# Kernel tuning notes

Measured on AMD Instinct MI355X. Metric: run time of the kernel, lower is better.

## Reference

```python
import jax, jax.numpy as jnp
import numpy as np
from jax import lax


def _nms(heat):
    # 3x3 max-pool, stride 1, SAME padding (torch pads with -inf for max pool)
    hmax = lax.reduce_window(heat, -jnp.inf, lax.max,
                             (1, 1, 3, 3), (1, 1, 1, 1), 'SAME')
    return jnp.where(hmax == heat, heat, jnp.zeros_like(heat))


def _decode(hmap, regs, w_h_, rot, K):
    B, C, H, W = hmap.shape
    heat = _nms(jax.nn.sigmoid(hmap))
    # stage 1: per-class top-k over the H*W spatial grid
    scores_flat = heat.reshape(B, C, H * W)
    topk_scores, topk_inds = lax.top_k(scores_flat, K)          # [B, C, K]
    topk_ys = (topk_inds // W).astype(heat.dtype)
    topk_xs = (topk_inds % W).astype(heat.dtype)
    # stage 2: top-k over all C*K candidates
    topk_score, topk_ind = lax.top_k(topk_scores.reshape(B, C * K), K)  # [B, K]
    clses = (topk_ind // K).astype(heat.dtype)                   # [B, K]
    inds = jnp.take_along_axis(topk_inds.reshape(B, C * K), topk_ind, axis=1)
    ys = jnp.take_along_axis(topk_ys.reshape(B, C * K), topk_ind, axis=1)
    xs = jnp.take_along_axis(topk_xs.reshape(B, C * K), topk_ind, axis=1)

    def gather_feat(feat):  # feat: [B, ch, H, W] -> [B, K, ch]
        ch = feat.shape[1]
        f = feat.transpose(0, 2, 3, 1).reshape(B, H * W, ch)
        return jnp.take_along_axis(f, inds[:, :, None], axis=1)

    regs_g = gather_feat(regs)   # [B, K, 2]
    wh_g = gather_feat(w_h_)     # [B, K, 2]
    rot_g = gather_feat(rot)     # [B, K, 1]
    xs = xs[:, :, None] + regs_g[:, :, 0:1]
    ys = ys[:, :, None] + regs_g[:, :, 1:2]
    # detections: [x, y, w, h, rot, score, cls] -> [B, K, 7]
    return jnp.concatenate(
        [xs, ys, wh_g, rot_g, topk_score[:, :, None], clses[:, :, None]], axis=2)


def setup_inputs() -> dict:
    key = jax.random.key(0)
    k1, k2, k3, k4 = jax.random.split(key, 4)
    B, C, H, W = 1, 80, 512, 512
    return {
        'hmap': jax.random.normal(k1, (B, C, H, W), dtype=jnp.float32),
        'regs': jax.random.normal(k2, (B, 2, H, W), dtype=jnp.float32),
        'w_h_': jax.random.uniform(k3, (B, 2, H, W), dtype=jnp.float32) * 64.0,
        'rot': jax.random.normal(k4, (B, 1, H, W), dtype=jnp.float32),
        'K': 100,
    }


def reference(hmap, regs, w_h_, rot, K):
    return _decode(hmap, regs, w_h_, rot, K)
```

## Files before the change

kernel.cpp:

```cpp
#include <hip/hip_runtime.h>
#include <cstdint>

#define HH 512
#define WW 512
#define HWSZ (HH * WW)
#define TILE_H 16
#define NSEG 128
#define SEGPAD 16
#define SEGCAP 256
#define FCAP 4096
#define T0F 3.75f
#define BINBASE 8248u
#define NVB 1024

__device__ __forceinline__ float sigmoid_f(float x) {
    return 1.0f / (1.0f + expf(-x));
}

__device__ __forceinline__ uint32_t vbin(uint32_t key) {
    uint32_t b = (key >> 17) - BINBASE;
    return b > (NVB - 1) ? (NVB - 1) : b;
}

__global__ __launch_bounds__(64) void main_pass(const float* __restrict__ hmap,
                                                int nTiles,
                                                uint32_t* __restrict__ segCount,
                                                uint2* __restrict__ cand) {
    int t = blockIdx.x;
    if (t >= nTiles) return;
    const int lane = threadIdx.x;
    const int cls = t >> 5;
    const int ty = t & 31;
    const int y0 = ty * TILE_H;
    const float* base = hmap + (size_t)cls * HWSZ;
    const int xA = lane * 4;
    const int xB = 256 + lane * 4;
    const int seg = t & (NSEG - 1);
    const float NEG = -__builtin_inff();

    float4 a0, a1, a2, b0, b1, b2;
    int rm1 = (y0 > 0) ? y0 - 1 : 0;
    a0 = *(const float4*)(base + rm1 * WW + xA);
    b0 = *(const float4*)(base + rm1 * WW + xB);
    a1 = *(const float4*)(base + y0 * WW + xA);
    b1 = *(const float4*)(base + y0 * WW + xB);

    #pragma unroll
    for (int r = 0; r < TILE_H; ++r) {
        int j = y0 + 1 + r;
        int jc = (j < HH) ? j : HH - 1;
        a2 = *(const float4*)(base + jc * WW + xA);
        b2 = *(const float4*)(base + jc * WW + xB);

        float cA = fmaxf(fmaxf(a1.x, a1.y), fmaxf(a1.z, a1.w));
        float cB = fmaxf(fmaxf(b1.x, b1.y), fmaxf(b1.z, b1.w));
        if (__any(fmaxf(cA, cB) >= T0F)) {
            float4 vA, vB;
            vA.x = fmaxf(fmaxf(a0.x, a1.x), a2.x);
            vA.y = fmaxf(fmaxf(a0.y, a1.y), a2.y);
            vA.z = fmaxf(fmaxf(a0.z, a1.z), a2.z);
            vA.w = fmaxf(fmaxf(a0.w, a1.w), a2.w);
            vB.x = fmaxf(fmaxf(b0.x, b1.x), b2.x);
            vB.y = fmaxf(fmaxf(b0.y, b1.y), b2.y);
            vB.z = fmaxf(fmaxf(b0.z, b1.z), b2.z);
            vB.w = fmaxf(fmaxf(b0.w, b1.w), b2.w);
            float vAl = __shfl_up(vA.w, 1);
            float vAr = __shfl_down(vA.x, 1);
            float vBl = __shfl_up(vB.w, 1);
            float vBr = __shfl_down(vB.x, 1);
            float seamR = __shfl(vB.x, 0);
            float seamL = __shfl(vA.w, 63);
            if (lane == 0)  { vAl = NEG; vBl = seamL; }
            if (lane == 63) { vAr = seamR; vBr = NEG; }
            float mA0 = fmaxf(fmaxf(vAl, vA.x), vA.y);
            float mA1 = fmaxf(fmaxf(vA.x, vA.y), vA.z);
            float mA2 = fmaxf(fmaxf(vA.y, vA.z), vA.w);
            float mA3 = fmaxf(fmaxf(vA.z, vA.w), vAr);
            float mB0 = fmaxf(fmaxf(vBl, vB.x), vB.y);
            float mB1 = fmaxf(fmaxf(vB.x, vB.y), vB.z);
            float mB2 = fmaxf(fmaxf(vB.y, vB.z), vB.w);
            float mB3 = fmaxf(fmaxf(vB.z, vB.w), vBr);

            int row = y0 + r;
            auto testc = [&](float c, float m, int col) {
                if (c >= T0F && (m <= c + 0.7f || c > 14.0f)) {
                    float s = sigmoid_f(c), sm = sigmoid_f(m);
                    if (s == sm) {
                        uint32_t slot = atomicAdd(&segCount[seg * SEGPAD], 1u);
                        if (slot < SEGCAP)
                            cand[seg * SEGCAP + slot] = make_uint2(
                                __float_as_uint(c),
                                (uint32_t)(cls * HWSZ + row * WW + col));
                    }
                }
            };
            testc(a1.x, mA0, xA + 0); testc(a1.y, mA1, xA + 1);
            testc(a1.z, mA2, xA + 2); testc(a1.w, mA3, xA + 3);
            testc(b1.x, mB0, xB + 0); testc(b1.y, mB1, xB + 1);
            testc(b1.z, mB2, xB + 2); testc(b1.w, mB3, xB + 3);
        }
        a0 = a1; a1 = a2; b0 = b1; b1 = b2;
    }
}

__global__ __launch_bounds__(256) void finalize_kernel(
        const uint2* __restrict__ cand, const uint32_t* __restrict__ segCount,
        const int* __restrict__ Kp, const float* __restrict__ hmap,
        const float* __restrict__ regs, const float* __restrict__ wh,
        const float* __restrict__ rot, int total, float* __restrict__ out) {
    __shared__ uint2 flat[FCAP];
    __shared__ uint32_t vhist[NVB];
    __shared__ uint32_t sOff[NSEG + 1];
    __shared__ uint32_t cnts[NSEG];
    __shared__ uint32_t chunkSum[128];
    __shared__ int sFlag, sN, sKept, sThr;

    int t = threadIdx.x;
    int K = *Kp;
    if (t == 0) { sFlag = 0; sKept = 0; }
    for (int i = t; i < NVB; i += 256) vhist[i] = 0;
    if (t < NSEG) {
        uint32_t c = segCount[t * SEGPAD];
        if (c > SEGCAP) { sFlag = 1; c = SEGCAP; }
        cnts[t] = c;
    }
    __syncthreads();
    if (t == 0) {
        uint32_t o = 0;
        for (int s = 0; s < NSEG; ++s) { sOff[s] = o; o += cnts[s]; }
        sOff[NSEG] = o;
        sN = (int)o;
        if ((int)o < K || o > FCAP) sFlag = 1;
    }
    __syncthreads();
    int flag = sFlag;
    int n;

    if (!flag) {
        n = sN;
        for (int k0 = t * 4; k0 < n; k0 += 1024) {
            uint2 r[4]; int kk[4]; int nv = 0;
            #pragma unroll
            for (int u = 0; u < 4; ++u) {
                int k = k0 + u;
                if (k < n) {
                    int lo = 0, hi = NSEG;
                    while (hi - lo > 1) {
                        int mid = (lo + hi) >> 1;
                        if (sOff[mid] <= (uint32_t)k) lo = mid; else hi = mid;
                    }
                    r[u] = cand[lo * SEGCAP + (k - (int)sOff[lo])];
                    kk[u] = k; nv = u + 1;
                }
            }
            #pragma unroll
            for (int u = 0; u < 4; ++u)
                if (u < nv) flat[kk[u]] = r[u];
        }
        __syncthreads();
    } else {
        for (int gid = t; gid < total; gid += 256) {
            float ctr = hmap[gid];
            if (ctr < T0F) continue;
            int pos = gid & (HWSZ - 1);
            int y = pos >> 9, x = pos & (WW - 1);
            const float* bse = hmap + (gid - pos);
            float m = ctr;
            int yl = y > 0 ? y - 1 : 0, yh = y < HH - 1 ? y + 1 : HH - 1;
            int xl = x > 0 ? x - 1 : 0, xh = x < WW - 1 ? x + 1 : WW - 1;
            for (int yy = yl; yy <= yh; ++yy)
                for (int xx = xl; xx <= xh; ++xx)
                    m = fmaxf(m, bse[yy * WW + xx]);
            float s = sigmoid_f(ctr), sm = sigmoid_f(m);
            if (s == sm) {
                int slot = atomicAdd(&sKept, 1);
                if (slot < FCAP) flat[slot] = make_uint2(__float_as_uint(ctr), (uint32_t)gid);
            }
        }
        __syncthreads();
        n = min(sKept, FCAP);
        __syncthreads();
        if (t == 0) sKept = 0;
    }

    for (int k = t; k < n; k += 256) atomicAdd(&vhist[vbin(flat[k].x)], 1u);
    __syncthreads();
    if (t < 128) {
        uint32_t s = 0;
        for (int i = 0; i < 8; ++i) s += vhist[t * 8 + i];
        chunkSum[t] = s;
    }
    __syncthreads();
    if (t == 0) {
        uint32_t cum = 0; int thr = 0; bool fnd = false;
        for (int c = 127; c >= 0 && !fnd; --c) {
            if (cum + chunkSum[c] >= (uint32_t)K) {
                for (int b = c * 8 + 7; b >= c * 8; --b) {
                    cum += vhist[b];
                    if (cum >= (uint32_t)K) { thr = b; fnd = true; break; }
                }
            } else cum += chunkSum[c];
        }
        sThr = fnd ? (thr > 0 ? thr - 1 : 0) : 0;
    }
    __syncthreads();
    uint32_t thrM1 = (uint32_t)sThr;

    for (int bse = 0; bse < n; bse += 256) {
        uint2 rec; bool keep = false;
        int k = bse + t;
        if (k < n) { rec = flat[k]; keep = vbin(rec.x) >= thrM1; }
        __syncthreads();
        if (keep) {
            float s = sigmoid_f(__uint_as_float(rec.x));
            int slot = atomicAdd(&sKept, 1);
            flat[slot] = make_uint2(__float_as_uint(s), rec.y);
        }
        __syncthreads();
    }
    int m = sKept;
    if (m > FCAP) m = FCAP;

    for (int i = t; i < m; i += 256) {
        uint2 me = flat[i];
        int rank = 0;
        for (int j = 0; j < m; ++j) {
            uint2 o = flat[j];
            rank += (int)((o.x > me.x) || (o.x == me.x && o.y < me.y));
        }
        if (rank < K) {
            int gid = (int)me.y;
            int cls = gid >> 18;
            int pos = gid & (HWSZ - 1);
            float yf = (float)(pos >> 9);
            float xf = (float)(pos & (WW - 1));
            float* o7 = out + rank * 7;
            o7[0] = xf + regs[pos];
            o7[1] = yf + regs[HWSZ + pos];
            o7[2] = wh[pos];
            o7[3] = wh[HWSZ + pos];
            o7[4] = rot[pos];
            o7[5] = __uint_as_float(me.x);
            o7[6] = (float)cls;
        }
    }
}

extern "C" void kernel_launch(void* const* d_in, const int* in_sizes, int n_in,
                              void* d_out, int out_size, void* d_ws, size_t ws_size,
                              hipStream_t stream) {
    const float* hmap = (const float*)d_in[0];
    const float* regs = (const float*)d_in[1];
    const float* wh   = (const float*)d_in[2];
    const float* rot  = (const float*)d_in[3];
    const int*   Kp   = (const int*)d_in[4];
    float* out = (float*)d_out;

    int total = in_sizes[0];
    int nTiles = (total / HWSZ) * (HH / TILE_H);

    uint32_t* ws = (uint32_t*)d_ws;
    uint32_t* segCount = ws;
    uint2* cand = (uint2*)(ws + NSEG * SEGPAD);

    hipMemsetAsync(d_ws, 0, (size_t)NSEG * SEGPAD * sizeof(uint32_t), stream);
    main_pass<<<nTiles, 64, 0, stream>>>(hmap, nTiles, segCount, cand);
    finalize_kernel<<<1, 256, 0, stream>>>(cand, segCount, Kp, hmap, regs, wh, rot,
                                           total, out);
}
```

Baseline: 155.1 us.

## Fuse scan and finalize into one kernel with last-block-done handoff

```diff
diff --git a/kernel.cpp b/kernel.cpp
--- a/kernel.cpp
+++ b/kernel.cpp
@@ -22,110 +22,124 @@
     return b > (NVB - 1) ? (NVB - 1) : b;
 }
 
-__global__ __launch_bounds__(64) void main_pass(const float* __restrict__ hmap,
-                                                int nTiles,
-                                                uint32_t* __restrict__ segCount,
-                                                uint2* __restrict__ cand) {
-    int t = blockIdx.x;
-    if (t >= nTiles) return;
-    const int lane = threadIdx.x;
-    const int cls = t >> 5;
-    const int ty = t & 31;
-    const int y0 = ty * TILE_H;
-    const float* base = hmap + (size_t)cls * HWSZ;
-    const int xA = lane * 4;
-    const int xB = 256 + lane * 4;
-    const int seg = t & (NSEG - 1);
-    const float NEG = -__builtin_inff();
-
-    float4 a0, a1, a2, b0, b1, b2;
-    int rm1 = (y0 > 0) ? y0 - 1 : 0;
-    a0 = *(const float4*)(base + rm1 * WW + xA);
-    b0 = *(const float4*)(base + rm1 * WW + xB);
-    a1 = *(const float4*)(base + y0 * WW + xA);
-    b1 = *(const float4*)(base + y0 * WW + xB);
-
-    #pragma unroll
-    for (int r = 0; r < TILE_H; ++r) {
-        int j = y0 + 1 + r;
-        int jc = (j < HH) ? j : HH - 1;
-        a2 = *(const float4*)(base + jc * WW + xA);
-        b2 = *(const float4*)(base + jc * WW + xB);
-
-        float cA = fmaxf(fmaxf(a1.x, a1.y), fmaxf(a1.z, a1.w));
-        float cB = fmaxf(fmaxf(b1.x, b1.y), fmaxf(b1.z, b1.w));
-        if (__any(fmaxf(cA, cB) >= T0F)) {
-            float4 vA, vB;
-            vA.x = fmaxf(fmaxf(a0.x, a1.x), a2.x);
-            vA.y = fmaxf(fmaxf(a0.y, a1.y), a2.y);
-            vA.z = fmaxf(fmaxf(a0.z, a1.z), a2.z);
-            vA.w = fmaxf(fmaxf(a0.w, a1.w), a2.w);
-            vB.x = fmaxf(fmaxf(b0.x, b1.x), b2.x);
-            vB.y = fmaxf(fmaxf(b0.y, b1.y), b2.y);
-            vB.z = fmaxf(fmaxf(b0.z, b1.z), b2.z);
-            vB.w = fmaxf(fmaxf(b0.w, b1.w), b2.w);
-            float vAl = __shfl_up(vA.w, 1);
-            float vAr = __shfl_down(vA.x, 1);
-            float vBl = __shfl_up(vB.w, 1);
-            float vBr = __shfl_down(vB.x, 1);
-            float seamR = __shfl(vB.x, 0);
-            float seamL = __shfl(vA.w, 63);
-            if (lane == 0)  { vAl = NEG; vBl = seamL; }
-            if (lane == 63) { vAr = seamR; vBr = NEG; }
-            float mA0 = fmaxf(fmaxf(vAl, vA.x), vA.y);
-            float mA1 = fmaxf(fmaxf(vA.x, vA.y), vA.z);
-            float mA2 = fmaxf(fmaxf(vA.y, vA.z), vA.w);
-            float mA3 = fmaxf(fmaxf(vA.z, vA.w), vAr);
-            float mB0 = fmaxf(fmaxf(vBl, vB.x), vB.y);
-            float mB1 = fmaxf(fmaxf(vB.x, vB.y), vB.z);
-            float mB2 = fmaxf(fmaxf(vB.y, vB.z), vB.w);
-            float mB3 = fmaxf(fmaxf(vB.z, vB.w), vBr);
-
-            int row = y0 + r;
-            auto testc = [&](float c, float m, int col) {
-                if (c >= T0F && (m <= c + 0.7f || c > 14.0f)) {
-                    float s = sigmoid_f(c), sm = sigmoid_f(m);
-                    if (s == sm) {
-                        uint32_t slot = atomicAdd(&segCount[seg * SEGPAD], 1u);
-                        if (slot < SEGCAP)
-                            cand[seg * SEGCAP + slot] = make_uint2(
-                                __float_as_uint(c),
-                                (uint32_t)(cls * HWSZ + row * WW + col));
-                    }
-                }
-            };
-            testc(a1.x, mA0, xA + 0); testc(a1.y, mA1, xA + 1);
-            testc(a1.z, mA2, xA + 2); testc(a1.w, mA3, xA + 3);
-            testc(b1.x, mB0, xB + 0); testc(b1.y, mB1, xB + 1);
-            testc(b1.z, mB2, xB + 2); testc(b1.w, mB3, xB + 3);
-        }
-        a0 = a1; a1 = a2; b0 = b1; b1 = b2;
-    }
-}
-
-__global__ __launch_bounds__(256) void finalize_kernel(
-        const uint2* __restrict__ cand, const uint32_t* __restrict__ segCount,
-        const int* __restrict__ Kp, const float* __restrict__ hmap,
+__global__ __launch_bounds__(256) void fused_pass(
+        const float* __restrict__ hmap, int nTiles, int total,
         const float* __restrict__ regs, const float* __restrict__ wh,
-        const float* __restrict__ rot, int total, float* __restrict__ out) {
+        const float* __restrict__ rot, const int* __restrict__ Kp,
+        uint32_t* __restrict__ segCount, uint32_t* __restrict__ done,
+        uint2* __restrict__ cand, float* __restrict__ out) {
     __shared__ uint2 flat[FCAP];
     __shared__ uint32_t vhist[NVB];
     __shared__ uint32_t sOff[NSEG + 1];
     __shared__ uint32_t cnts[NSEG];
     __shared__ uint32_t chunkSum[128];
-    __shared__ int sFlag, sN, sKept, sThr;
-
-    int t = threadIdx.x;
+    __shared__ int sFlag, sN, sKept, sThr, sLast;
+
+    const int t256 = threadIdx.x;
+    const int lane = t256 & 63;
+    const int wv = t256 >> 6;
+    const int tile = blockIdx.x * 4 + wv;
+    const float NEG = -__builtin_inff();
+
+    if (tile < nTiles) {
+        const int cls = tile >> 5;
+        const int ty = tile & 31;
+        const int y0 = ty * TILE_H;
+        const float* base = hmap + (size_t)cls * HWSZ;
+        const int xA = lane * 4;
+        const int xB = 256 + lane * 4;
+        const int seg = tile & (NSEG - 1);
+
+        float4 A0, A1, A2, A3, B0, B1, B2, B3;
+        int rm1 = (y0 > 0) ? y0 - 1 : 0;
+        A0 = *(const float4*)(base + rm1 * WW + xA);
+        B0 = *(const float4*)(base + rm1 * WW + xB);
+        A1 = *(const float4*)(base + y0 * WW + xA);
+        B1 = *(const float4*)(base + y0 * WW + xB);
+        int r1 = (y0 + 1 < HH) ? y0 + 1 : HH - 1;
+        A2 = *(const float4*)(base + r1 * WW + xA);
+        B2 = *(const float4*)(base + r1 * WW + xB);
+        A3 = A2; B3 = B2;
+
+        #pragma unroll
+        for (int r = 0; r < TILE_H; ++r) {
+            if (r < TILE_H - 1) {
+                int j = y0 + 2 + r;
+                int jc = (j < HH) ? j : HH - 1;
+                A3 = *(const float4*)(base + jc * WW + xA);
+                B3 = *(const float4*)(base + jc * WW + xB);
+            }
+            float cA = fmaxf(fmaxf(A1.x, A1.y), fmaxf(A1.z, A1.w));
+            float cB = fmaxf(fmaxf(B1.x, B1.y), fmaxf(B1.z, B1.w));
+            if (__any(fmaxf(cA, cB) >= T0F)) {
+                float4 vA, vB;
+                vA.x = fmaxf(fmaxf(A0.x, A1.x), A2.x);
+                vA.y = fmaxf(fmaxf(A0.y, A1.y), A2.y);
+                vA.z = fmaxf(fmaxf(A0.z, A1.z), A2.z);
+                vA.w = fmaxf(fmaxf(A0.w, A1.w), A2.w);
+                vB.x = fmaxf(fmaxf(B0.x, B1.x), B2.x);
+                vB.y = fmaxf(fmaxf(B0.y, B1.y), B2.y);
+                vB.z = fmaxf(fmaxf(B0.z, B1.z), B2.z);
+                vB.w = fmaxf(fmaxf(B0.w, B1.w), B2.w);
+                float vAl = __shfl_up(vA.w, 1);
+                float vAr = __shfl_down(vA.x, 1);
+                float vBl = __shfl_up(vB.w, 1);
+                float vBr = __shfl_down(vB.x, 1);
+                float seamR = __shfl(vB.x, 0);
+                float seamL = __shfl(vA.w, 63);
+                if (lane == 0)  { vAl = NEG; vBl = seamL; }
+                if (lane == 63) { vAr = seamR; vBr = NEG; }
+                float mA0 = fmaxf(fmaxf(vAl, vA.x), vA.y);
+                float mA1 = fmaxf(fmaxf(vA.x, vA.y), vA.z);
+                float mA2 = fmaxf(fmaxf(vA.y, vA.z), vA.w);
+                float mA3 = fmaxf(fmaxf(vA.z, vA.w), vAr);
+                float mB0 = fmaxf(fmaxf(vBl, vB.x), vB.y);
+                float mB1 = fmaxf(fmaxf(vB.x, vB.y), vB.z);
+                float mB2 = fmaxf(fmaxf(vB.y, vB.z), vB.w);
+                float mB3 = fmaxf(fmaxf(vB.z, vB.w), vBr);
+
+                int row = y0 + r;
+                auto testc = [&](float c, float m, int col) {
+                    if (c >= T0F && (m <= c + 0.7f || c > 14.0f)) {
+                        float s = sigmoid_f(c), sm = sigmoid_f(m);
+                        if (s == sm) {
+                            uint32_t slot = atomicAdd(&segCount[seg * SEGPAD], 1u);
+                            if (slot < SEGCAP)
+                                cand[seg * SEGCAP + slot] = make_uint2(
+                                    __float_as_uint(c),
+                                    (uint32_t)(cls * HWSZ + row * WW + col));
+                        }
+                    }
+                };
+                testc(A1.x, mA0, xA + 0); testc(A1.y, mA1, xA + 1);
+                testc(A1.z, mA2, xA + 2); testc(A1.w, mA3, xA + 3);
+                testc(B1.x, mB0, xB + 0); testc(B1.y, mB1, xB + 1);
+                testc(B1.z, mB2, xB + 2); testc(B1.w, mB3, xB + 3);
+            }
+            A0 = A1; A1 = A2; A2 = A3; B0 = B1; B1 = B2; B2 = B3;
+        }
+    }
+
+    __threadfence();
+    __syncthreads();
+    if (t256 == 0) {
+        uint32_t old = atomicAdd(done, 1u);
+        sLast = (old == gridDim.x - 1) ? 1 : 0;
+    }
+    __syncthreads();
+    if (!sLast) return;
+    __threadfence();
+
     int K = *Kp;
-    if (t == 0) { sFlag = 0; sKept = 0; }
-    for (int i = t; i < NVB; i += 256) vhist[i] = 0;
-    if (t < NSEG) {
-        uint32_t c = segCount[t * SEGPAD];
+    if (t256 == 0) { sFlag = 0; sKept = 0; }
+    for (int i = t256; i < NVB; i += 256) vhist[i] = 0;
+    if (t256 < NSEG) {
+        uint32_t c = segCount[t256 * SEGPAD];
         if (c > SEGCAP) { sFlag = 1; c = SEGCAP; }
-        cnts[t] = c;
-    }
-    __syncthreads();
-    if (t == 0) {
+        cnts[t256] = c;
+    }
+    __syncthreads();
+    if (t256 == 0) {
         uint32_t o = 0;
         for (int s = 0; s < NSEG; ++s) { sOff[s] = o; o += cnts[s]; }
         sOff[NSEG] = o;
@@ -138,7 +152,7 @@
 
     if (!flag) {
         n = sN;
-        for (int k0 = t * 4; k0 < n; k0 += 1024) {
+        for (int k0 = t256 * 4; k0 < n; k0 += 1024) {
             uint2 r[4]; int kk[4]; int nv = 0;
             #pragma unroll
             for (int u = 0; u < 4; ++u) {
@@ -159,7 +173,7 @@
         }
         __syncthreads();
     } else {
-        for (int gid = t; gid < total; gid += 256) {
+        for (int gid = t256; gid < total; gid += 256) {
             float ctr = hmap[gid];
             if (ctr < T0F) continue;
             int pos = gid & (HWSZ - 1);
@@ -180,18 +194,18 @@
         __syncthreads();
         n = min(sKept, FCAP);
         __syncthreads();
-        if (t == 0) sKept = 0;
-    }
-
-    for (int k = t; k < n; k += 256) atomicAdd(&vhist[vbin(flat[k].x)], 1u);
-    __syncthreads();
-    if (t < 128) {
+        if (t256 == 0) sKept = 0;
+    }
+
+    for (int k = t256; k < n; k += 256) atomicAdd(&vhist[vbin(flat[k].x)], 1u);
+    __syncthreads();
+    if (t256 < 128) {
         uint32_t s = 0;
-        for (int i = 0; i < 8; ++i) s += vhist[t * 8 + i];
-        chunkSum[t] = s;
-    }
-    __syncthreads();
-    if (t == 0) {
+        for (int i = 0; i < 8; ++i) s += vhist[t256 * 8 + i];
+        chunkSum[t256] = s;
+    }
+    __syncthreads();
+    if (t256 == 0) {
         uint32_t cum = 0; int thr = 0; bool fnd = false;
         for (int c = 127; c >= 0 && !fnd; --c) {
             if (cum + chunkSum[c] >= (uint32_t)K) {
@@ -208,7 +222,7 @@
 
     for (int bse = 0; bse < n; bse += 256) {
         uint2 rec; bool keep = false;
-        int k = bse + t;
+        int k = bse + t256;
         if (k < n) { rec = flat[k]; keep = vbin(rec.x) >= thrM1; }
         __syncthreads();
         if (keep) {
@@ -221,7 +235,7 @@
     int m = sKept;
     if (m > FCAP) m = FCAP;
 
-    for (int i = t; i < m; i += 256) {
+    for (int i = t256; i < m; i += 256) {
         uint2 me = flat[i];
         int rank = 0;
         for (int j = 0; j < m; ++j) {
@@ -258,13 +272,14 @@
 
     int total = in_sizes[0];
     int nTiles = (total / HWSZ) * (HH / TILE_H);
+    int nBlocks = (nTiles + 3) / 4;
 
     uint32_t* ws = (uint32_t*)d_ws;
     uint32_t* segCount = ws;
-    uint2* cand = (uint2*)(ws + NSEG * SEGPAD);
-
-    hipMemsetAsync(d_ws, 0, (size_t)NSEG * SEGPAD * sizeof(uint32_t), stream);
-    main_pass<<<nTiles, 64, 0, stream>>>(hmap, nTiles, segCount, cand);
-    finalize_kernel<<<1, 256, 0, stream>>>(cand, segCount, Kp, hmap, regs, wh, rot,
-                                           total, out);
-}
+    uint32_t* done = ws + 2048;
+    uint2* cand = (uint2*)(ws + 2064);
+
+    hipMemsetAsync(d_ws, 0, 2064 * sizeof(uint32_t), stream);
+    fused_pass<<<nBlocks, 256, 0, stream>>>(hmap, nTiles, total, regs, wh, rot, Kp,
+                                            segCount, done, cand, out);
+}
```

Result: slower. 252.8 us (+62.9%).
